# Kernel tuning notes

Hardware: AMD Instinct MI355X
Metric: run time of the kernel (lower is better)

The kernel has to match this reference:

```python
import jax, jax.numpy as jnp
import numpy as np

H = 1024  # hidden_size


def setup_inputs() -> dict:
    key = jax.random.key(0)
    ks = jax.random.split(key, 8)
    B, S = 32, 2048
    scale_w = 1.0 / np.sqrt(H)
    scale_u = 1.0 / np.sqrt(2 * H)
    return {
        "encoder_annotations": jax.random.normal(ks[0], (B, S, 2 * H), dtype=jnp.float32),
        "decoder_prev_hidden": jax.random.normal(ks[1], (1, B, H), dtype=jnp.float32),
        "W_w": jax.random.uniform(ks[2], (H, H), jnp.float32, -scale_w, scale_w),
        "W_b": jax.random.uniform(ks[3], (H,), jnp.float32, -scale_w, scale_w),
        "U_w": jax.random.uniform(ks[4], (H, 2 * H), jnp.float32, -scale_u, scale_u),
        "U_b": jax.random.uniform(ks[5], (H,), jnp.float32, -scale_u, scale_u),
        "V_w": jax.random.uniform(ks[6], (1, H), jnp.float32, -scale_w, scale_w),
        "V_b": jax.random.uniform(ks[7], (1,), jnp.float32, -scale_w, scale_w),
    }


def reference(encoder_annotations, decoder_prev_hidden, W_w, W_b, U_w, U_b, V_w, V_b):
    # decoder_prev_hidden: [1, B, H] -> [B, 1, H]
    dh = jnp.transpose(decoder_prev_hidden, (1, 0, 2))
    # W(dh): [B, 1, H]; U(enc): [B, S, H]; broadcast add over S
    wq = jnp.einsum("boh,kh->bok", dh, W_w) + W_b
    uk = jnp.einsum("bsd,kd->bsk", encoder_annotations, U_w) + U_b
    act = jnp.tanh(wq + uk)  # [B, S, H]
    # V(act): [B, S, 1] -> scores [B, 1, S]
    scores = (jnp.einsum("bsh,oh->bso", act, V_w) + V_b).transpose(0, 2, 1)
    weights = jax.nn.softmax(scores, axis=2)  # [B, 1, S]
    context = jnp.einsum("bos,sd->bod", weights[:, 0:1].squeeze(1)[:, None, :].squeeze(1)[:, None, :], encoder_annotations) if False else jnp.matmul(weights, encoder_annotations)  # [B, 1, 2H]
    return context
```

## Files before the change

### kernel.cpp

```cpp
#include <hip/hip_runtime.h>
#include <hip/hip_bf16.h>

#define H_  1024
#define B_  32
#define S_  2048
#define K2_ 2048

typedef __attribute__((ext_vector_type(8))) short short8;
typedef __attribute__((ext_vector_type(4))) float floatx4;
typedef __attribute__((ext_vector_type(8))) unsigned short ushortx8;

__device__ __forceinline__ unsigned short f2bf(float x) {
    unsigned int u = __float_as_uint(x);
    u += 0x7fffu + ((u >> 16) & 1u);
    return (unsigned short)(u >> 16);
}

__device__ __forceinline__ float fast_tanh(float x) {
    float e = __expf(2.0f * x);
    return 1.0f - 2.0f / (e + 1.0f);
}

__device__ __forceinline__ void gload_lds16(const void* g, void* l) {
    __builtin_amdgcn_global_load_lds(
        (const __attribute__((address_space(1))) unsigned int*)g,
        (__attribute__((address_space(3))) unsigned int*)l, 16, 0, 0);
}

__global__ __launch_bounds__(256)
void cvt_bf16_k(const float* __restrict__ in, unsigned short* __restrict__ out, long long n8)
{
    long long i = (long long)blockIdx.x * 256 + threadIdx.x;
    long long stride = (long long)gridDim.x * 256;
    for (; i < n8; i += stride) {
        const float4* p = (const float4*)in + i * 2;
        float4 a = p[0], b = p[1];
        ushortx8 o = { f2bf(a.x), f2bf(a.y), f2bf(a.z), f2bf(a.w),
                       f2bf(b.x), f2bf(b.y), f2bf(b.z), f2bf(b.w) };
        *(ushortx8*)(out + i * 8) = o;
    }
}

__global__ __launch_bounds__(256)
void wq_k(const float* __restrict__ dh, const float* __restrict__ Ww,
          const float* __restrict__ Wb, const float* __restrict__ Ub,
          float* __restrict__ wqbuf)
{
    const int b = blockIdx.y;
    const int n = blockIdx.x * 256 + threadIdx.x;
    const int tid = threadIdx.x;
    __shared__ float dhs[H_];
    for (int h = tid; h < H_; h += 256) dhs[h] = dh[b * H_ + h];
    __syncthreads();
    const float4* row = (const float4*)(Ww + (size_t)n * H_);
    float acc = 0.f;
    #pragma unroll 4
    for (int h4 = 0; h4 < H_ / 4; h4++) {
        float4 wv = row[h4];
        acc += wv.x * dhs[h4 * 4 + 0] + wv.y * dhs[h4 * 4 + 1]
             + wv.z * dhs[h4 * 4 + 2] + wv.w * dhs[h4 * 4 + 3];
    }
    wqbuf[b * H_ + n] = acc + Wb[n] + Ub[n];
}

__global__ __launch_bounds__(256)
void gemm_scores_bf16(const unsigned short* __restrict__ encb,
                      const unsigned short* __restrict__ Uwb,
                      const float* __restrict__ wqbuf, const float* __restrict__ Vw,
                      float* __restrict__ partial)
{
    const int b   = blockIdx.z;
    const int mt  = blockIdx.x;
    const int nt  = blockIdx.y;
    const int tid = threadIdx.x;
    const int wave = tid >> 6;
    const int lane = tid & 63;

    __shared__ unsigned short As[128 * 32];
    __shared__ unsigned short Bs[128 * 32];
    __shared__ float sc[2][128];

    const unsigned short* Ag = encb + ((size_t)b * S_ + (size_t)mt * 128) * K2_;
    const unsigned short* Bg = Uwb + (size_t)nt * 128 * K2_;

    floatx4 acc[4][4];
    #pragma unroll
    for (int i = 0; i < 4; i++)
        #pragma unroll
        for (int j = 0; j < 4; j++)
            acc[i][j] = (floatx4){0.f, 0.f, 0.f, 0.f};

    const int wm  = (wave & 1) * 64;
    const int wn  = (wave >> 1) * 64;
    const int l15 = lane & 15;
    const int kq  = (lane >> 4) * 8;

    const int r0 = lane >> 2;
    const int ke = (lane & 3) * 8;
    const unsigned short* aptr = Ag + (size_t)(wave * 32 + r0) * K2_ + ke;
    const unsigned short* bptr = Bg + (size_t)(wave * 32 + r0) * K2_ + ke;
    unsigned short* AldsA = As + wave * 1024;
    unsigned short* AldsB = Bs + wave * 1024;

    for (int ks = 0; ks < K2_; ks += 32) {
        gload_lds16(aptr + ks,             AldsA);
        gload_lds16(aptr + 16 * K2_ + ks,  AldsA + 512);
        gload_lds16(bptr + ks,             AldsB);
        gload_lds16(bptr + 16 * K2_ + ks,  AldsB + 512);
        __syncthreads();

        short8 af[4], bfr[4];
        #pragma unroll
        for (int t = 0; t < 4; t++) {
            af[t]  = *(const short8*)&As[(wm + t * 16 + l15) * 32 + kq];
            bfr[t] = *(const short8*)&Bs[(wn + t * 16 + l15) * 32 + kq];
        }
        #pragma unroll
        for (int tm = 0; tm < 4; tm++)
            #pragma unroll
            for (int tn = 0; tn < 4; tn++)
                acc[tm][tn] = __builtin_amdgcn_mfma_f32_16x16x32_bf16(
                    af[tm], bfr[tn], acc[tm][tn], 0, 0, 0);
        __syncthreads();
    }

    float rs[4][4];
    #pragma unroll
    for (int tm = 0; tm < 4; tm++)
        #pragma unroll
        for (int r = 0; r < 4; r++) rs[tm][r] = 0.f;

    #pragma unroll
    for (int tn = 0; tn < 4; tn++) {
        int ng = nt * 128 + wn + tn * 16 + l15;
        float vw = Vw[ng];
        float wv = wqbuf[b * H_ + ng];
        #pragma unroll
        for (int tm = 0; tm < 4; tm++)
            #pragma unroll
            for (int r = 0; r < 4; r++)
                rs[tm][r] += vw * fast_tanh(acc[tm][tn][r] + wv);
    }
    #pragma unroll
    for (int tm = 0; tm < 4; tm++)
        #pragma unroll
        for (int r = 0; r < 4; r++) {
            float v = rs[tm][r];
            v += __shfl_xor(v, 1, 64);
            v += __shfl_xor(v, 2, 64);
            v += __shfl_xor(v, 4, 64);
            v += __shfl_xor(v, 8, 64);
            rs[tm][r] = v;
        }
    if (l15 == 0) {
        int q = lane >> 4;
        #pragma unroll
        for (int tm = 0; tm < 4; tm++)
            #pragma unroll
            for (int r = 0; r < 4; r++)
                sc[wave >> 1][wm + tm * 16 + q * 4 + r] = rs[tm][r];
    }
    __syncthreads();
    if (tid < 128)
        partial[(size_t)(b * 8 + nt) * S_ + mt * 128 + tid] = sc[0][tid] + sc[1][tid];
}

__global__ __launch_bounds__(256)
void gemm_scores_f32(const float* __restrict__ enc, const float* __restrict__ Uw,
                     const float* __restrict__ wqbuf, const float* __restrict__ Vw,
                     float* __restrict__ partial)
{
    const int b   = blockIdx.z;
    const int mt  = blockIdx.x;
    const int nt  = blockIdx.y;
    const int tid = threadIdx.x;
    const int wave = tid >> 6;
    const int lane = tid & 63;

    __shared__ unsigned short As[128][32];
    __shared__ unsigned short Bs[128][32];
    __shared__ float sc[2][128];

    const float* Ab = enc + ((size_t)b * S_ + (size_t)mt * 128) * K2_;
    const float* Bb = Uw + (size_t)nt * 128 * K2_;

    floatx4 acc[4][4];
    #pragma unroll
    for (int i = 0; i < 4; i++)
        #pragma unroll
        for (int j = 0; j < 4; j++)
            acc[i][j] = (floatx4){0.f, 0.f, 0.f, 0.f};

    const int wm  = (wave & 1) * 64;
    const int wn  = (wave >> 1) * 64;
    const int l15 = lane & 15;
    const int kq  = (lane >> 4) * 8;

    for (int ks = 0; ks < K2_; ks += 32) {
        #pragma unroll
        for (int i = 0; i < 4; i++) {
            int lin = tid + 256 * i;
            int row = lin >> 3;
            int kk  = (lin & 7) << 2;
            float4 av = *(const float4*)(Ab + (size_t)row * K2_ + ks + kk);
            float4 bv = *(const float4*)(Bb + (size_t)row * K2_ + ks + kk);
            ushort4 a4 = { f2bf(av.x), f2bf(av.y), f2bf(av.z), f2bf(av.w) };
            ushort4 b4 = { f2bf(bv.x), f2bf(bv.y), f2bf(bv.z), f2bf(bv.w) };
            *(ushort4*)&As[row][kk] = a4;
            *(ushort4*)&Bs[row][kk] = b4;
        }
        __syncthreads();

        short8 af[4], bfr[4];
        #pragma unroll
        for (int t = 0; t < 4; t++) {
            af[t]  = *(const short8*)&As[wm + t * 16 + l15][kq];
            bfr[t] = *(const short8*)&Bs[wn + t * 16 + l15][kq];
        }
        #pragma unroll
        for (int tm = 0; tm < 4; tm++)
            #pragma unroll
            for (int tn = 0; tn < 4; tn++)
                acc[tm][tn] = __builtin_amdgcn_mfma_f32_16x16x32_bf16(
                    af[tm], bfr[tn], acc[tm][tn], 0, 0, 0);
        __syncthreads();
    }

    float rs[4][4];
    #pragma unroll
    for (int tm = 0; tm < 4; tm++)
        #pragma unroll
        for (int r = 0; r < 4; r++) rs[tm][r] = 0.f;

    #pragma unroll
    for (int tn = 0; tn < 4; tn++) {
        int ng = nt * 128 + wn + tn * 16 + l15;
        float vw = Vw[ng];
        float wv = wqbuf[b * H_ + ng];
        #pragma unroll
        for (int tm = 0; tm < 4; tm++)
            #pragma unroll
            for (int r = 0; r < 4; r++)
                rs[tm][r] += vw * fast_tanh(acc[tm][tn][r] + wv);
    }
    #pragma unroll
    for (int tm = 0; tm < 4; tm++)
        #pragma unroll
        for (int r = 0; r < 4; r++) {
            float v = rs[tm][r];
            v += __shfl_xor(v, 1, 64);
            v += __shfl_xor(v, 2, 64);
            v += __shfl_xor(v, 4, 64);
            v += __shfl_xor(v, 8, 64);
            rs[tm][r] = v;
        }
    if (l15 == 0) {
        int q = lane >> 4;
        #pragma unroll
        for (int tm = 0; tm < 4; tm++)
            #pragma unroll
            for (int r = 0; r < 4; r++)
                sc[wave >> 1][wm + tm * 16 + q * 4 + r] = rs[tm][r];
    }
    __syncthreads();
    if (tid < 128)
        partial[(size_t)(b * 8 + nt) * S_ + mt * 128 + tid] = sc[0][tid] + sc[1][tid];
}

__global__ __launch_bounds__(256)
void softmax_k(const float* __restrict__ partial, float* __restrict__ weights)
{
    const int b = blockIdx.x;
    const int tid = threadIdx.x;
    __shared__ float scores[S_];
    __shared__ float redm[4], reds[4];

    for (int s = tid; s < S_; s += 256) {
        float v = 0.f;
        #pragma unroll
        for (int nt = 0; nt < 8; nt++) v += partial[(size_t)(b * 8 + nt) * S_ + s];
        scores[s] = v;
    }
    __syncthreads();

    float m = -1e30f;
    for (int s = tid; s < S_; s += 256) m = fmaxf(m, scores[s]);
    #pragma unroll
    for (int off = 32; off > 0; off >>= 1) m = fmaxf(m, __shfl_xor(m, off, 64));
    if ((tid & 63) == 0) redm[tid >> 6] = m;
    __syncthreads();
    m = fmaxf(fmaxf(redm[0], redm[1]), fmaxf(redm[2], redm[3]));

    float sum = 0.f;
    for (int s = tid; s < S_; s += 256) {
        float e = __expf(scores[s] - m);
        scores[s] = e;
        sum += e;
    }
    #pragma unroll
    for (int off = 32; off > 0; off >>= 1) sum += __shfl_xor(sum, off, 64);
    if ((tid & 63) == 0) reds[tid >> 6] = sum;
    __syncthreads();
    sum = reds[0] + reds[1] + reds[2] + reds[3];
    float inv = 1.0f / sum;
    for (int s = tid; s < S_; s += 256) weights[b * S_ + s] = scores[s] * inv;
}

__global__ __launch_bounds__(256)
void context2_k(const float* __restrict__ enc, const float* __restrict__ weights,
                float* __restrict__ pctx)
{
    const int b = blockIdx.z, scnk = blockIdx.y, dblk = blockIdx.x;
    const int tid = threadIdx.x;
    __shared__ float w[256];
    w[tid] = weights[b * S_ + scnk * 256 + tid];
    __syncthreads();

    const float4* e = (const float4*)(enc + ((size_t)b * S_ + scnk * 256) * K2_)
                      + dblk * 256 + tid;
    float4 a0 = {0,0,0,0}, a1 = {0,0,0,0};
    #pragma unroll 4
    for (int s = 0; s < 256; s += 2) {
        float4 v0 = e[(size_t)s * 512];
        float4 v1 = e[(size_t)(s + 1) * 512];
        float w0 = w[s], w1 = w[s + 1];
        a0.x += w0 * v0.x; a0.y += w0 * v0.y; a0.z += w0 * v0.z; a0.w += w0 * v0.w;
        a1.x += w1 * v1.x; a1.y += w1 * v1.y; a1.z += w1 * v1.z; a1.w += w1 * v1.w;
    }
    float4 acc = { a0.x + a1.x, a0.y + a1.y, a0.z + a1.z, a0.w + a1.w };
    float4* o = (float4*)(pctx + (size_t)(b * 8 + scnk) * K2_) + dblk * 256 + tid;
    *o = acc;
}

__global__ __launch_bounds__(256)
void ctx_reduce_k(const float* __restrict__ pctx, float* __restrict__ out)
{
    const int i = blockIdx.x * 256 + threadIdx.x;
    const int b = i >> 11, d = i & 2047;
    float s = 0.f;
    #pragma unroll
    for (int c = 0; c < 8; c++) s += pctx[(size_t)(b * 8 + c) * K2_ + d];
    out[i] = s;
}

extern "C" void kernel_launch(void* const* d_in, const int* in_sizes, int n_in,
                              void* d_out, int out_size, void* d_ws, size_t ws_size,
                              hipStream_t stream)
{
    const float* enc = (const float*)d_in[0];
    const float* dh  = (const float*)d_in[1];
    const float* Ww  = (const float*)d_in[2];
    const float* Wb  = (const float*)d_in[3];
    const float* Uw  = (const float*)d_in[4];
    const float* Ub  = (const float*)d_in[5];
    const float* Vw  = (const float*)d_in[6];
    float* out = (float*)d_out;

    float* wqbuf   = (float*)d_ws;
    float* partial = wqbuf + B_ * H_;
    float* weights = partial + B_ * 8 * S_;
    float* pctx    = weights + B_ * S_;
    size_t small_bytes = (size_t)(B_*H_ + B_*8*S_ + B_*S_ + B_*8*S_) * 4;
    unsigned short* Uwb  = (unsigned short*)((char*)d_ws + small_bytes);
    unsigned short* encb = Uwb + (size_t)H_ * K2_;
    size_t need = small_bytes + (size_t)H_ * K2_ * 2 + (size_t)B_ * S_ * K2_ * 2;

    wq_k<<<dim3(4, B_), dim3(256), 0, stream>>>(dh, Ww, Wb, Ub, wqbuf);

    if (ws_size >= need) {
        long long n8_enc = (long long)B_ * S_ * K2_ / 8;
        long long n8_uw  = (long long)H_ * K2_ / 8;
        cvt_bf16_k<<<dim3(8192), dim3(256), 0, stream>>>(enc, encb, n8_enc);
        cvt_bf16_k<<<dim3(1024), dim3(256), 0, stream>>>(Uw, Uwb, n8_uw);
        gemm_scores_bf16<<<dim3(16, 8, B_), dim3(256), 0, stream>>>(encb, Uwb, wqbuf, Vw, partial);
    } else {
        gemm_scores_f32<<<dim3(16, 8, B_), dim3(256), 0, stream>>>(enc, Uw, wqbuf, Vw, partial);
    }

    softmax_k<<<dim3(B_), dim3(256), 0, stream>>>(partial, weights);
    context2_k<<<dim3(2, 8, B_), dim3(256), 0, stream>>>(enc, weights, pctx);
    ctx_reduce_k<<<dim3(256), dim3(256), 0, stream>>>(pctx, out);
}
```

Before: 1.211 ms.

## Double-buffer LDS tiles with swizzled layout in scores GEMM

Splits the shared-memory A/B tiles into two buffers so the global-to-LDS loads for the next K-step are issued before the MFMA work on the current step, using explicit vmcnt waits and barriers instead of __syncthreads. It also XOR-swizzles the 16-byte chunk position within each row to reduce LDS bank conflicts on the fragment reads. The aim is to hide global load latency and LDS conflicts in the main GEMM loop, at the cost of doubled LDS use, which may lower occupancy, and more fragile hand-written wait counts.

```diff
diff --git a/kernel.cpp b/kernel.cpp
--- a/kernel.cpp
+++ b/kernel.cpp
@@ -76,8 +76,8 @@
     const int wave = tid >> 6;
     const int lane = tid & 63;
 
-    __shared__ unsigned short As[128 * 32];
-    __shared__ unsigned short Bs[128 * 32];
+    __shared__ unsigned short As[2][128 * 32];
+    __shared__ unsigned short Bs[2][128 * 32];
     __shared__ float sc[2][128];
 
     const unsigned short* Ag = encb + ((size_t)b * S_ + (size_t)mt * 128) * K2_;
@@ -93,36 +93,56 @@
     const int wm  = (wave & 1) * 64;
     const int wn  = (wave >> 1) * 64;
     const int l15 = lane & 15;
-    const int kq  = (lane >> 4) * 8;
-
-    const int r0 = lane >> 2;
-    const int ke = (lane & 3) * 8;
-    const unsigned short* aptr = Ag + (size_t)(wave * 32 + r0) * K2_ + ke;
-    const unsigned short* bptr = Bg + (size_t)(wave * 32 + r0) * K2_ + ke;
-    unsigned short* AldsA = As + wave * 1024;
-    unsigned short* AldsB = Bs + wave * 1024;
-
-    for (int ks = 0; ks < K2_; ks += 32) {
-        gload_lds16(aptr + ks,             AldsA);
-        gload_lds16(aptr + 16 * K2_ + ks,  AldsA + 512);
-        gload_lds16(bptr + ks,             AldsB);
-        gload_lds16(bptr + 16 * K2_ + ks,  AldsB + 512);
-        __syncthreads();
-
-        short8 af[4], bfr[4];
-        #pragma unroll
-        for (int t = 0; t < 4; t++) {
-            af[t]  = *(const short8*)&As[(wm + t * 16 + l15) * 32 + kq];
-            bfr[t] = *(const short8*)&Bs[(wn + t * 16 + l15) * 32 + kq];
-        }
-        #pragma unroll
-        for (int tm = 0; tm < 4; tm++)
-            #pragma unroll
-            for (int tn = 0; tn < 4; tn++)
-                acc[tm][tn] = __builtin_amdgcn_mfma_f32_16x16x32_bf16(
-                    af[tm], bfr[tn], acc[tm][tn], 0, 0, 0);
-        __syncthreads();
-    }
+
+    const int r_in = lane >> 2;
+    const int ch   = (lane & 3) ^ (r_in & 3);
+    const unsigned short* aptr = Ag + (size_t)(wave * 32 + r_in) * K2_ + ch * 8;
+    const unsigned short* bptr = Bg + (size_t)(wave * 32 + r_in) * K2_ + ch * 8;
+
+    const int cq   = lane >> 4;
+    const int slot = (cq ^ (l15 & 3)) << 3;
+
+#define STAGE(bs, ks) do {                                         \
+        unsigned short* _ad = &As[bs][wave * 1024];                \
+        unsigned short* _bd = &Bs[bs][wave * 1024];                \
+        gload_lds16(aptr + (ks),            _ad);                  \
+        gload_lds16(aptr + 16 * K2_ + (ks), _ad + 512);            \
+        gload_lds16(bptr + (ks),            _bd);                  \
+        gload_lds16(bptr + 16 * K2_ + (ks), _bd + 512);            \
+    } while (0)
+
+#define COMPUTE(bs) do {                                                        \
+        short8 af[4], bfr[4];                                                   \
+        _Pragma("unroll")                                                       \
+        for (int t = 0; t < 4; t++) {                                           \
+            af[t]  = *(const short8*)&As[bs][(wm + t * 16 + l15) * 32 + slot];  \
+            bfr[t] = *(const short8*)&Bs[bs][(wn + t * 16 + l15) * 32 + slot];  \
+        }                                                                       \
+        _Pragma("unroll")                                                       \
+        for (int tm = 0; tm < 4; tm++)                                          \
+            _Pragma("unroll")                                                   \
+            for (int tn = 0; tn < 4; tn++)                                      \
+                acc[tm][tn] = __builtin_amdgcn_mfma_f32_16x16x32_bf16(          \
+                    af[tm], bfr[tn], acc[tm][tn], 0, 0, 0);                     \
+    } while (0)
+
+    STAGE(0, 0);
+    int cur = 0;
+    for (int t = 0; t < 63; ++t) {
+        STAGE(cur ^ 1, (t + 1) * 32);
+        asm volatile("s_waitcnt vmcnt(4)" ::: "memory");
+        __builtin_amdgcn_s_barrier();
+        COMPUTE(cur);
+        asm volatile("s_waitcnt lgkmcnt(0)" ::: "memory");
+        __builtin_amdgcn_s_barrier();
+        cur ^= 1;
+    }
+    asm volatile("s_waitcnt vmcnt(0)" ::: "memory");
+    __builtin_amdgcn_s_barrier();
+    COMPUTE(cur);
+
+#undef STAGE
+#undef COMPUTE
 
     float rs[4][4];
     #pragma unroll
```

Result: slower. 1.319 ms (+8.9%).
